# Performance work log

Measured on AMD Instinct MI355X. Metric: run time of the kernel, lower is better.

## Reference

```python
import jax, jax.numpy as jnp
import numpy as np

DIM = 256
RATIO = 4
SCALE = 8
B, H, W = 16, 128, 128
EPS = 1e-5


def _conv(x, w, pad):
    return jax.lax.conv_general_dilated(
        x, w, window_strides=(1, 1), padding=[(pad, pad), (pad, pad)],
        dimension_numbers=('NCHW', 'OIHW', 'NCHW'))


def _haar_dwt(x):
    # pywt.dwt2(x, 'haar') on even-sized inputs == strided 2x2 sum/difference
    a = x[:, :, 0::2, 0::2]
    b = x[:, :, 0::2, 1::2]
    c = x[:, :, 1::2, 0::2]
    d = x[:, :, 1::2, 1::2]
    ll = (a + b + c + d) * 0.5
    lh = (a + b - c - d) * 0.5  # cH: high-pass along rows
    hl = (a - b + c - d) * 0.5  # cV: high-pass along cols
    hh = (a - b - c + d) * 0.5  # cD
    return jnp.concatenate([ll, lh, hl, hh], axis=1)


def setup_inputs() -> dict:
    key = jax.random.key(0)
    ks = jax.random.split(key, 16)
    dq = DIM // RATIO
    ds = DIM // SCALE
    s = 0.05
    return {
        'x': jax.random.normal(ks[0], (B, DIM, H, W), jnp.float32),
        'reduce_w': jax.random.normal(ks[1], (dq, DIM, 1, 1), jnp.float32) * s,
        'reduce_b': jnp.zeros((dq,), jnp.float32),
        'bn_g': jnp.ones((dq,), jnp.float32),
        'bn_b': jnp.zeros((dq,), jnp.float32),
        'bn_mean': jnp.zeros((dq,), jnp.float32),
        'bn_var': jnp.ones((dq,), jnp.float32),
        'conv_w': jax.random.normal(ks[2], (1, DIM, 1, 1), jnp.float32) * s,
        'conv1_w': jax.random.normal(ks[3], (DIM, DIM, 1, 1), jnp.float32) * s,
        'conv2_w': jax.random.normal(ks[4], (DIM, DIM, 3, 3), jnp.float32) * s,
        'conv3_w': jax.random.normal(ks[5], (DIM, DIM, 5, 5), jnp.float32) * s,
        'conv4_w': jax.random.normal(ks[6], (DIM, DIM, 7, 7), jnp.float32) * s,
        'channel_conv_w': jax.random.normal(ks[7], (DIM, DIM, 3, 3), jnp.float32) * s,
        'conv1x1_w': jax.random.normal(ks[8], (DIM, 6 * DIM, 3, 3), jnp.float32) * s,
        'ct1_w': jax.random.normal(ks[9], (ds, DIM, 1, 1), jnp.float32) * s,
        'ct1_b': jnp.zeros((ds,), jnp.float32),
        'ln_g': jnp.ones((ds,), jnp.float32),
        'ln_b': jnp.zeros((ds,), jnp.float32),
        'ct2_w': jax.random.normal(ks[10], (DIM, ds, 1, 1), jnp.float32) * s,
        'ct2_b': jnp.zeros((DIM,), jnp.float32),
        'proj_w': jax.random.normal(ks[11], (DIM, DIM, 1, 1), jnp.float32) * s,
    }


def reference(x, reduce_w, reduce_b, bn_g, bn_b, bn_mean, bn_var, conv_w,
              conv1_w, conv2_w, conv3_w, conv4_w, channel_conv_w, conv1x1_w,
              ct1_w, ct1_b, ln_g, ln_b, ct2_w, ct2_b, proj_w):
    # max-pool 2x2 stride 2
    p = jax.lax.reduce_window(x, -jnp.inf, jax.lax.max,
                              (1, 1, 2, 2), (1, 1, 2, 2), 'VALID')
    # reduce: 1x1 conv -> BN (inference) -> ReLU
    r = _conv(x, reduce_w, 0) + reduce_b[None, :, None, None]
    r = (r - bn_mean[None, :, None, None]) * jax.lax.rsqrt(bn_var + EPS)[None, :, None, None]
    r = jax.nn.relu(r * bn_g[None, :, None, None] + bn_b[None, :, None, None])
    # Haar DWT (original runs under no_grad: detached from autograd)
    qkv0 = jax.lax.stop_gradient(_haar_dwt(r))  # [B, DIM, H/2, W/2]
    qkv1 = _conv(qkv0, conv1_w, 0)
    qkv2 = _conv(qkv0, conv2_w, 1)
    qkv3 = _conv(qkv0, conv3_w, 2)
    qkv4 = _conv(qkv0, conv4_w, 3)
    qkv = _conv(jnp.concatenate([qkv0, qkv1, qkv2, qkv3, qkv4, p], axis=1),
                conv1x1_w, 1)  # [B, DIM, H/2, W/2]
    n = (H // 2) * (W // 2)
    # spatial attention weights: softmax over spatial positions
    content = _conv(qkv, conv_w, 0).reshape(B, n)          # [B, N]
    content = jax.nn.softmax(content, axis=1)
    channel = _conv(qkv, channel_conv_w, 1).reshape(B, DIM, n)  # [B, C, N]
    pooled = jnp.einsum('bcn,bn->bc', channel, content)[:, :, None, None]
    # channel transform: 1x1 -> LayerNorm over (C,1,1) -> ReLU -> 1x1
    t = _conv(pooled, ct1_w, 0) + ct1_b[None, :, None, None]
    mu = jnp.mean(t, axis=(1, 2, 3), keepdims=True)
    var = jnp.mean(jnp.square(t - mu), axis=(1, 2, 3), keepdims=True)
    t = (t - mu) * jax.lax.rsqrt(var + EPS)
    t = jax.nn.relu(t * ln_g[None, :, None, None] + ln_b[None, :, None, None])
    cw = _conv(t, ct2_w, 0) + ct2_b[None, :, None, None]  # [B, DIM, 1, 1]
    return _conv(qkv * cw, proj_w, 0)
```

## Files before the change

kernel.cpp:

```cpp
#include <hip/hip_runtime.h>
#include <stdint.h>


typedef __attribute__((ext_vector_type(8))) short bf16x8;
typedef __attribute__((ext_vector_type(4))) float f32x4;

#define EPS_ 1e-5f

#define GLOAD16(gp, lp)                                                        \
  __builtin_amdgcn_global_load_lds(                                            \
      (const __attribute__((address_space(1))) void*)(gp),                     \
      (__attribute__((address_space(3))) void*)(lp), 16, 0, 0)

__device__ __forceinline__ float bf2f(unsigned short u) {
  union { unsigned int u; float f; } c; c.u = ((unsigned int)u) << 16; return c.f;
}
__device__ __forceinline__ unsigned short f2bf(float f) {
  union { float f; unsigned int u; } c; c.f = f;
  return (unsigned short)((c.u + 0x7fffu + ((c.u >> 16) & 1u)) >> 16);
}
__device__ __forceinline__ void unpack8(uint4 v, float* f) {
  f[0]=bf2f((unsigned short)(v.x&0xffffu)); f[1]=bf2f((unsigned short)(v.x>>16));
  f[2]=bf2f((unsigned short)(v.y&0xffffu)); f[3]=bf2f((unsigned short)(v.y>>16));
  f[4]=bf2f((unsigned short)(v.z&0xffffu)); f[5]=bf2f((unsigned short)(v.z>>16));
  f[6]=bf2f((unsigned short)(v.w&0xffffu)); f[7]=bf2f((unsigned short)(v.w>>16));
}
__device__ __forceinline__ uint4 pack8(const float* f) {
  uint4 v;
  v.x = (unsigned)f2bf(f[0]) | ((unsigned)f2bf(f[1])<<16);
  v.y = (unsigned)f2bf(f[2]) | ((unsigned)f2bf(f[3])<<16);
  v.z = (unsigned)f2bf(f[4]) | ((unsigned)f2bf(f[5])<<16);
  v.w = (unsigned)f2bf(f[6]) | ((unsigned)f2bf(f[7])<<16);
  return v;
}

__global__ void k_repack(const float* __restrict__ src, unsigned short* __restrict__ dst,
                         int O, int Opad, int I, int T) {
  int gid = blockIdx.x * 256 + threadIdx.x;
  if (gid >= Opad * I * T) return;
  int i = gid % I; int r = gid / I; int o = r % Opad; int t = r / Opad;
  dst[gid] = (o < O) ? f2bf(src[((size_t)(o * I + i)) * T + t]) : (unsigned short)0;
}

__global__ void k_fold1(const float* __restrict__ catw, const float* __restrict__ w1,
                        unsigned short* __restrict__ dst) {
  int gid = blockIdx.x; int tid = threadIdx.x;
  int iq = gid % 5; int o = (gid / 5) & 255; int t = gid / 1280;
  int i = iq * 256 + tid;
  float s;
  if (i < 256) {
    s = catw[((size_t)o * 1536 + i) * 9 + t];
    const float* cw = catw + ((size_t)o * 1536 + 256) * 9 + t;
    for (int m = 0; m < 256; ++m)
      s += cw[(size_t)m * 9] * w1[m * 256 + i];
  } else {
    s = catw[((size_t)o * 1536 + i + 256) * 9 + t];
  }
  dst[((size_t)t * 256 + o) * 1280 + i] = f2bf(s);
}

__global__ void k_border_zero(unsigned short* __restrict__ buf, int PW, int PB, int C) {
  int IW = PW - 2 * PB;
  int nb = PW * PW - IW * IW;
  int per = C >> 3;
  int gid = blockIdx.x * 256 + threadIdx.x;
  if (gid >= 16 * nb * per) return;
  int cq = gid % per; int r = gid / per; int p = r % nb; int b = r / nb;
  int y, x;
  int top = PB * PW;
  if (p < top) { y = p / PW; x = p - y * PW; }
  else if (p < top + IW * 2 * PB) {
    int q = p - top; y = PB + q / (2 * PB); int rr = q % (2 * PB);
    x = (rr < PB) ? rr : (IW + rr);
  } else { int q = p - top - IW * 2 * PB; y = PB + IW + q / PW; x = q - (q / PW) * PW; }
  uint4 z; z.x = z.y = z.z = z.w = 0u;
  *(uint4*)&buf[(((size_t)b * PW + y) * PW + x) * C + cq * 8] = z;
}

__global__ void k_transpose_x(const float* __restrict__ x, unsigned short* __restrict__ xh) {
  int by = blockIdx.x; int b = by >> 7; int y = by & 127;
  int tid = threadIdx.x;
  __shared__ unsigned short lds[32 * 129];
  for (int c0 = 0; c0 < 256; c0 += 32) {
    #pragma unroll
    for (int i = 0; i < 16; ++i) {
      int e = i * 256 + tid; int ci = e >> 7, xx = e & 127;
      float v = x[(((size_t)b * 256 + c0 + ci) * 128 + y) * 128 + xx];
      lds[ci * 129 + xx] = f2bf(v);
    }
    __syncthreads();
    #pragma unroll
    for (int i2 = 0; i2 < 2; ++i2) {
      int e = i2 * 256 + tid; int pix = e >> 2, q = e & 3;
      unsigned int w0, w1, w2, w3;
      w0 = (unsigned)lds[(q*8+0)*129 + pix] | ((unsigned)lds[(q*8+1)*129 + pix] << 16);
      w1 = (unsigned)lds[(q*8+2)*129 + pix] | ((unsigned)lds[(q*8+3)*129 + pix] << 16);
      w2 = (unsigned)lds[(q*8+4)*129 + pix] | ((unsigned)lds[(q*8+5)*129 + pix] << 16);
      w3 = (unsigned)lds[(q*8+6)*129 + pix] | ((unsigned)lds[(q*8+7)*129 + pix] << 16);
      uint4 v; v.x = w0; v.y = w1; v.z = w2; v.w = w3;
      *(uint4*)&xh[(((size_t)b * 128 + y) * 128 + pix) * 256 + c0 + q * 8] = v;
    }
    __syncthreads();
  }
}

__global__ void k_maxpool(const unsigned short* __restrict__ xh, unsigned short* __restrict__ cat) {
  int gid = blockIdx.x * 256 + threadIdx.x;
  int cq = gid & 31; int pix = gid >> 5;
  int bb = pix >> 12; int yx = pix & 4095;
  int y = yx >> 6, xx2 = yx & 63;
  size_t base = (((size_t)bb * 128 + 2 * y) * 128 + 2 * xx2) * 256 + cq * 8;
  uint4 v00 = *(const uint4*)(xh + base);
  uint4 v01 = *(const uint4*)(xh + base + 256);
  uint4 v10 = *(const uint4*)(xh + base + 32768);
  uint4 v11 = *(const uint4*)(xh + base + 32768 + 256);
  float a[8], b8[8], c8[8], d8[8], m8[8];
  unpack8(v00, a); unpack8(v01, b8); unpack8(v10, c8); unpack8(v11, d8);
  #pragma unroll
  for (int j = 0; j < 8; ++j) m8[j] = fmaxf(fmaxf(a[j], b8[j]), fmaxf(c8[j], d8[j]));
  *(uint4*)(cat + (((size_t)bb * 4900 + (y + 3) * 70 + (xx2 + 3))) * 1280 + 1024 + cq * 8) = pack8(m8);
}

__global__ void k_haar(const unsigned short* __restrict__ rbn, unsigned short* __restrict__ cat) {
  int gid = blockIdx.x * 256 + threadIdx.x;
  int cq = gid & 7; int pix = gid >> 3;
  int bb = pix >> 12; int yx = pix & 4095;
  int y = yx >> 6, xx = yx & 63;
  size_t base = (((size_t)bb * 128 + 2 * y) * 128 + 2 * xx) * 64 + cq * 8;
  uint4 va = *(const uint4*)(rbn + base);
  uint4 vb = *(const uint4*)(rbn + base + 64);
  uint4 vc = *(const uint4*)(rbn + base + 8192);
  uint4 vd = *(const uint4*)(rbn + base + 8192 + 64);
  float a[8], b8[8], c8[8], d8[8], o[8];
  unpack8(va, a); unpack8(vb, b8); unpack8(vc, c8); unpack8(vd, d8);
  size_t ob = ((size_t)bb * 4900 + (y + 3) * 70 + (xx + 3)) * 1280 + cq * 8;
  #pragma unroll
  for (int j = 0; j < 8; ++j) o[j] = (a[j] + b8[j] + c8[j] + d8[j]) * 0.5f;
  *(uint4*)(cat + ob + 0)   = pack8(o);
  #pragma unroll
  for (int j = 0; j < 8; ++j) o[j] = (a[j] + b8[j] - c8[j] - d8[j]) * 0.5f;
  *(uint4*)(cat + ob + 64)  = pack8(o);
  #pragma unroll
  for (int j = 0; j < 8; ++j) o[j] = (a[j] - b8[j] + c8[j] - d8[j]) * 0.5f;
  *(uint4*)(cat + ob + 128) = pack8(o);
  #pragma unroll
  for (int j = 0; j < 8; ++j) o[j] = (a[j] - b8[j] - c8[j] + d8[j]) * 0.5f;
  *(uint4*)(cat + ob + 192) = pack8(o);
}

__global__ __launch_bounds__(512, 1) void k_conv_gemm256(
    const unsigned short* __restrict__ Wt, const unsigned short* __restrict__ Bf,
    int Cin, int Cstr, int cbase,
    int PW, int PB, int KH, int pad,
    unsigned long long wbstride,
    unsigned short* __restrict__ outb, int OCstr, int ocbase, int OPW, int OPB,
    float* __restrict__ outf, int mode) {
  const int tid = threadIdx.x, lane = tid & 63, w = tid >> 6;
  const int wm = w >> 2, wn = w & 3;
  const int nidx = (blockIdx.x & 7) * 32 + (blockIdx.x >> 3);
  const int bn = (nidx & 15) * 256;
  const int b = nidx >> 4;
  if (wbstride) Wt += (size_t)b * wbstride;
  extern __shared__ unsigned short S[];

  f32x4 zero4 = {0.f, 0.f, 0.f, 0.f};
  f32x4 acc[8][4];
  #pragma unroll
  for (int i = 0; i < 8; ++i)
    #pragma unroll
    for (int j = 0; j < 4; ++j) acc[i][j] = zero4;

  const int lq = lane >> 3, lc = lane & 7;
  const int lg = (lc - lq) & 7;
  const int pr = lg >> 2;
  const int ks = lg & 3;
  const unsigned short* aSt = Wt + (size_t)(w * 32 + 2 * lq + pr) * Cin + ks * 8;
  const size_t jA = (size_t)16 * Cin;
  const size_t bimg = (size_t)b * PW * PW;
  const unsigned short* bSt0; const unsigned short* bSt1;
  {
    int p = bn + w * 32 + 2 * lq + pr;
    bSt0 = Bf + (bimg + (size_t)((p >> 6) + PB) * PW + ((p & 63) + PB)) * Cstr + cbase + ks * 8;
    p += 16;
    bSt1 = Bf + (bimg + (size_t)((p >> 6) + PB) * PW + ((p & 63) + PB)) * Cstr + cbase + ks * 8;
  }
  const int dA = w * 1024;
  const int dB = 8192 + w * 1024;

  const int r = lane & 15, s4 = lane >> 4;
  const int ck = (((r & 1) * 4 + s4) + ((r >> 1) & 7)) & 7;
  const int lb = (r >> 1) * 64 + ck * 8;
  const int aOff = wm * 4096 + lb;
  const int bOff = 8192 + wn * 2048 + lb;

  const size_t MC = (size_t)256 * Cin;
  const int NT = (KH * KH * Cin) >> 5;

  const long long t0B = ((long long)(-pad) * PW + (-pad)) * (long long)Cstr;
  GLOAD16(aSt,             S + dA);
  GLOAD16(aSt + jA,        S + dA + 512);
  GLOAD16(bSt0 + t0B,      S + dB);
  GLOAD16(bSt1 + t0B,      S + dB + 512);
  GLOAD16(aSt + 32,        S + 16384 + dA);
  GLOAD16(aSt + jA + 32,   S + 16384 + dA + 512);
  GLOAD16(bSt0 + t0B + 32, S + 16384 + dB);
  GLOAD16(bSt1 + t0B + 32, S + 16384 + dB + 512);
  asm volatile("s_waitcnt vmcnt(4)" ::: "memory");
  __builtin_amdgcn_s_barrier();
  __builtin_amdgcn_sched_barrier(0);

  int kc2 = 64, ty2 = 0, tx2 = 0;
  for (int t = 0; t < NT; ++t) {
    const unsigned short* Sc = S + (t & 3) * 16384;
    unsigned short* Sn = (unsigned short*)S + ((t + 2) & 3) * 16384;
    const bool hn = (t + 2) < NT;
    long long offA = 0, offB = 0;
    if (hn) {
      offA = (long long)(ty2 * KH + tx2) * MC + kc2;
      offB = ((long long)(ty2 - pad) * PW + (tx2 - pad)) * (long long)Cstr + kc2;
      kc2 += 32;
      if (kc2 == Cin) { kc2 = 0; ++tx2; if (tx2 == KH) { tx2 = 0; ++ty2; } }
    }
    bf16x8 a[4], bb[4];
    #pragma unroll
    for (int mi = 0; mi < 4; ++mi) a[mi] = *(const bf16x8*)(Sc + aOff + mi * 512);
    #pragma unroll
    for (int ni = 0; ni < 4; ++ni) bb[ni] = *(const bf16x8*)(Sc + bOff + ni * 512);
    if (hn) {
      GLOAD16(aSt + offA,      Sn + dA);
      GLOAD16(aSt + jA + offA, Sn + dA + 512);
    }
    __builtin_amdgcn_s_setprio(1);
    #pragma unroll
    for (int mi = 0; mi < 4; ++mi)
      #pragma unroll
      for (int ni = 0; ni < 4; ++ni)
        acc[mi][ni] = __builtin_amdgcn_mfma_f32_16x16x32_bf16(a[mi], bb[ni], acc[mi][ni], 0, 0, 0);
    __builtin_amdgcn_s_setprio(0);
    __builtin_amdgcn_s_barrier();
    #pragma unroll
    for (int mi = 0; mi < 4; ++mi) a[mi] = *(const bf16x8*)(Sc + aOff + (mi + 4) * 512);
    if (hn) {
      GLOAD16(bSt0 + offB, Sn + dB);
      GLOAD16(bSt1 + offB, Sn + dB + 512);
    }
    __builtin_amdgcn_s_setprio(1);
    #pragma unroll
    for (int mi = 0; mi < 4; ++mi)
      #pragma unroll
      for (int ni = 0; ni < 4; ++ni)
        acc[mi + 4][ni] = __builtin_amdgcn_mfma_f32_16x16x32_bf16(a[mi], bb[ni], acc[mi + 4][ni], 0, 0, 0);
    __builtin_amdgcn_s_setprio(0);
    if (t + 1 < NT) {
      if (t + 2 < NT) { asm volatile("s_waitcnt vmcnt(4)" ::: "memory"); }
      else            { asm volatile("s_waitcnt vmcnt(0)" ::: "memory"); }
      __builtin_amdgcn_s_barrier();
      __builtin_amdgcn_sched_barrier(0);
    }
  }

  const size_t bimgO = (size_t)b * OPW * OPW;
  #pragma unroll
  for (int mi = 0; mi < 8; ++mi) {
    const int mf = wm * 128 + mi * 16 + (lane >> 4) * 4;
    #pragma unroll
    for (int ni = 0; ni < 4; ++ni) {
      const int n = bn + wn * 64 + ni * 16 + (lane & 15);
      if (mode == 2) {
        #pragma unroll
        for (int vv = 0; vv < 4; ++vv)
          outf[((size_t)b * 256 + mf + vv) * 4096 + n] = acc[mi][ni][vv];
      } else {
        const int oy = n >> 6, ox = n & 63;
        unsigned short h[4];
        #pragma unroll
        for (int vv = 0; vv < 4; ++vv) h[vv] = f2bf(acc[mi][ni][vv]);
        uint2 st; st.x = (unsigned)h[0] | ((unsigned)h[1] << 16);
        st.y = (unsigned)h[2] | ((unsigned)h[3] << 16);
        *(uint2*)&outb[(bimgO + (size_t)(oy + OPB) * OPW + (ox + OPB)) * OCstr + ocbase + mf] = st;
      }
    }
  }
}

__global__ __launch_bounds__(256) void k_conv_gemm(
    const unsigned short* __restrict__ Wt, const unsigned short* __restrict__ Bf,
    int M, int Mpad, int Cin, int Cstr, int cbase,
    int OW, int lgOW, int PW, int PB, int KH, int pad,
    unsigned long long wbstride,
    unsigned short* __restrict__ outb, int OCstr, int ocbase, int OPW, int OPB,
    float* __restrict__ outf, int mode,
    const float* __restrict__ rb, const float* __restrict__ bng, const float* __restrict__ bnb,
    const float* __restrict__ bnm, const float* __restrict__ bnv) {
  const int tid = threadIdx.x, lane = tid & 63, w = tid >> 6;
  const int wm = w >> 1, wn = w & 1;
  const int bm = blockIdx.y * 128, bn = blockIdx.x * 128;
  const int b = blockIdx.z;
  const int Npix = OW * OW;
  if (wbstride) Wt += (size_t)b * wbstride;

  __shared__ __align__(1024) unsigned short sA[128 * 32];
  __shared__ __align__(1024) unsigned short sB[128 * 32];

  f32x4 zero4 = {0.f, 0.f, 0.f, 0.f};
  f32x4 acc[4][4];
  #pragma unroll
  for (int i = 0; i < 4; ++i)
    #pragma unroll
    for (int j = 0; j < 4; ++j) acc[i][j] = zero4;

  const int srow = lane >> 2;
  const int slog = (lane & 3) ^ ((lane >> 3) & 3);
  const int r0 = w * 32;
  const unsigned short* aRow = Wt + ((size_t)(bm + r0 + srow)) * Cin + slog * 8;
  const int n0 = bn + r0 + srow, n1 = n0 + 16;
  const int y0 = n0 >> lgOW, x0 = n0 & (OW - 1);
  const int y1 = n1 >> lgOW, x1 = n1 & (OW - 1);
  const size_t bimg = (size_t)b * PW * PW;
  const unsigned short* bRow0 = Bf + (bimg + (size_t)(y0 + PB) * PW + (x0 + PB)) * Cstr + cbase + slog * 8;
  const unsigned short* bRow1 = Bf + (bimg + (size_t)(y1 + PB) * PW + (x1 + PB)) * Cstr + cbase + slog * 8;
  unsigned short* ldsA0 = &sA[(r0) * 32];
  unsigned short* ldsA1 = &sA[(r0 + 16) * 32];
  unsigned short* ldsB0 = &sB[(r0) * 32];
  unsigned short* ldsB1 = &sB[(r0 + 16) * 32];

  const int rowfrag = lane & 15, hi = lane >> 4;
  const int sl = hi ^ ((rowfrag >> 1) & 3);
  const bf16x8* pA[4]; const bf16x8* pB[4];
  #pragma unroll
  for (int mi = 0; mi < 4; ++mi)
    pA[mi] = (const bf16x8*)&sA[(wm * 64 + mi * 16 + rowfrag) * 32 + sl * 8];
  #pragma unroll
  for (int ni = 0; ni < 4; ++ni)
    pB[ni] = (const bf16x8*)&sB[(wn * 64 + ni * 16 + rowfrag) * 32 + sl * 8];

  const size_t MC = (size_t)Mpad * Cin;
  for (int ty = 0; ty < KH; ++ty) {
    for (int tx = 0; tx < KH; ++tx) {
      const unsigned short* at = aRow + (size_t)(ty * KH + tx) * MC;
      const long long toff = ((long long)(ty - pad) * PW + (tx - pad)) * Cstr;
      const unsigned short* bt0 = bRow0 + toff;
      const unsigned short* bt1 = bRow1 + toff;
      for (int kc = 0; kc < Cin; kc += 32) {
        GLOAD16(at + kc, ldsA0);
        GLOAD16(at + (size_t)16 * Cin + kc, ldsA1);
        GLOAD16(bt0 + kc, ldsB0);
        GLOAD16(bt1 + kc, ldsB1);
        __syncthreads();
        bf16x8 af[4], bfr[4];
        #pragma unroll
        for (int mi = 0; mi < 4; ++mi) af[mi] = *pA[mi];
        #pragma unroll
        for (int ni = 0; ni < 4; ++ni) bfr[ni] = *pB[ni];
        #pragma unroll
        for (int mi = 0; mi < 4; ++mi)
          #pragma unroll
          for (int ni = 0; ni < 4; ++ni)
            acc[mi][ni] = __builtin_amdgcn_mfma_f32_16x16x32_bf16(af[mi], bfr[ni], acc[mi][ni], 0, 0, 0);
        __syncthreads();
      }
    }
  }

  const int mb0 = bm + wm * 64, nb0 = bn + wn * 64;
  const size_t bimgO = (size_t)b * OPW * OPW;
  #pragma unroll
  for (int mi = 0; mi < 4; ++mi) {
    const int mf = mb0 + mi * 16 + (lane >> 4) * 4;
    if (mf >= M) continue;
    #pragma unroll
    for (int ni = 0; ni < 4; ++ni) {
      const int n = nb0 + ni * 16 + (lane & 15);
      if (mode == 2) {
        #pragma unroll
        for (int vv = 0; vv < 4; ++vv)
          outf[((size_t)b * M + mf + vv) * Npix + n] = acc[mi][ni][vv];
      } else {
        const int oy = n >> lgOW, ox = n & (OW - 1);
        unsigned short h[4];
        #pragma unroll
        for (int vv = 0; vv < 4; ++vv) {
          float val = acc[mi][ni][vv];
          if (mode == 1) {
            int m = mf + vv;
            float scl = bng[m] * rsqrtf(bnv[m] + EPS_);
            val = (val + rb[m] - bnm[m]) * scl + bnb[m];
            val = fmaxf(val, 0.f);
          }
          h[vv] = f2bf(val);
        }
        uint2 st; st.x = (unsigned)h[0] | ((unsigned)h[1] << 16);
        st.y = (unsigned)h[2] | ((unsigned)h[3] << 16);
        *(uint2*)&outb[(bimgO + (size_t)(oy + OPB) * OPW + (ox + OPB)) * OCstr + ocbase + mf] = st;
      }
    }
  }
}

__global__ void k_content_logits(const unsigned short* __restrict__ qkv,
                                 const float* __restrict__ conv_w,
                                 float* __restrict__ logits) {
  int j = blockIdx.x, b = blockIdx.y, tid = threadIdx.x;
  __shared__ float wl[256];
  wl[tid] = conv_w[tid];
  __syncthreads();
  int pl = tid >> 3, kp = tid & 7;
  #pragma unroll
  for (int pass = 0; pass < 4; ++pass) {
    int p = j * 128 + pass * 32 + pl;
    int y = p >> 6, x = p & 63;
    const unsigned short* q = qkv + (((size_t)b * 66 + y + 1) * 66 + (x + 1)) * 256 + kp * 32;
    float s = 0.f;
    #pragma unroll
    for (int i = 0; i < 32; i += 8) {
      uint4 v = *(const uint4*)(q + i);
      float f[8]; unpack8(v, f);
      #pragma unroll
      for (int k = 0; k < 8; ++k) s += f[k] * wl[kp * 32 + i + k];
    }
    s += __shfl_down(s, 4, 8);
    s += __shfl_down(s, 2, 8);
    s += __shfl_down(s, 1, 8);
    if (kp == 0) logits[(size_t)b * 4096 + p] = s;
  }
}

__global__ void k_softmax4096(float* __restrict__ cont) {
  int b = blockIdx.x, tid = threadIdx.x;
  __shared__ float red[256];
  float sv[16]; float mx = -1e30f;
  #pragma unroll
  for (int j = 0; j < 16; ++j) { sv[j] = cont[(size_t)b * 4096 + j * 256 + tid]; mx = fmaxf(mx, sv[j]); }
  red[tid] = mx; __syncthreads();
  for (int s = 128; s > 0; s >>= 1) { if (tid < s) red[tid] = fmaxf(red[tid], red[tid + s]); __syncthreads(); }
  mx = red[0]; __syncthreads();
  float sum = 0.f;
  #pragma unroll
  for (int j = 0; j < 16; ++j) { sv[j] = expf(sv[j] - mx); sum += sv[j]; }
  red[tid] = sum; __syncthreads();
  for (int s = 128; s > 0; s >>= 1) { if (tid < s) red[tid] += red[tid + s]; __syncthreads(); }
  float inv = 1.f / red[0];
  #pragma unroll
  for (int j = 0; j < 16; ++j) cont[(size_t)b * 4096 + j * 256 + tid] = sv[j] * inv;
}

__global__ void k_corr(const unsigned short* __restrict__ qkv,
                       const float* __restrict__ cont, float* __restrict__ gpart) {
  int j = blockIdx.x, b = blockIdx.y, i = threadIdx.x;
  __shared__ float cl[640];
  for (int e = i; e < 640; e += 256) {
    int gy = j * 8 - 1 + (e >> 6);
    cl[e] = (gy >= 0 && gy < 64) ? cont[(size_t)b * 4096 + gy * 64 + (e & 63)] : 0.f;
  }
  __syncthreads();
  float g[9] = {0.f, 0.f, 0.f, 0.f, 0.f, 0.f, 0.f, 0.f, 0.f};
  for (int ry = 0; ry < 8; ++ry) {
    int y = j * 8 + ry;
    for (int x = 0; x < 64; ++x) {
      float qv = bf2f(qkv[(((size_t)b * 66 + y + 1) * 66 + (x + 1)) * 256 + i]);
      #pragma unroll
      for (int ky = 0; ky < 3; ++ky) {
        int ly = ry - ky + 2;
        #pragma unroll
        for (int kx = 0; kx < 3; ++kx) {
          int nx = x - kx + 1;
          if ((unsigned)nx < 64u) g[ky * 3 + kx] += qv * cl[ly * 64 + nx];
        }
      }
    }
  }
  size_t base = ((size_t)b * 8 + j) * 2304 + i;
  #pragma unroll
  for (int t = 0; t < 9; ++t) gpart[base + t * 256] = g[t];
}

__global__ void k_pooled_g(const float* __restrict__ gpart,
                           const float* __restrict__ wc, float* __restrict__ pooled) {
  int b = blockIdx.x, c = threadIdx.x;
  __shared__ float Gs[2304];
  for (int e = c; e < 2304; e += 256) {
    float s = 0.f;
    #pragma unroll
    for (int j = 0; j < 8; ++j) s += gpart[((size_t)b * 8 + j) * 2304 + e];
    Gs[e] = s;
  }
  __syncthreads();
  float acc = 0.f;
  const float* w = wc + (size_t)c * 2304;
  for (int i = 0; i < 256; ++i)
    #pragma unroll
    for (int t = 0; t < 9; ++t)
      acc += w[i * 9 + t] * Gs[t * 256 + i];
  pooled[b * 256 + c] = acc;
}

__global__ void k_ct(const float* __restrict__ pooled,
                     const float* __restrict__ ct1w, const float* __restrict__ ct1b,
                     const float* __restrict__ lng, const float* __restrict__ lnb,
                     const float* __restrict__ ct2w, const float* __restrict__ ct2b,
                     float* __restrict__ cw) {
  int b = blockIdx.x, tid = threadIdx.x;
  __shared__ float tt[32];
  __shared__ float stats[2];
  if (tid < 32) {
    float s = 0.f;
    const float* w = ct1w + tid * 256;
    const float* p = pooled + b * 256;
    for (int i = 0; i < 256; ++i) s += w[i] * p[i];
    tt[tid] = s + ct1b[tid];
  }
  __syncthreads();
  if (tid == 0) {
    float mu = 0.f;
    for (int j = 0; j < 32; ++j) mu += tt[j];
    mu *= (1.f / 32.f);
    float va = 0.f;
    for (int j = 0; j < 32; ++j) { float d = tt[j] - mu; va += d * d; }
    va *= (1.f / 32.f);
    stats[0] = mu; stats[1] = rsqrtf(va + EPS_);
  }
  __syncthreads();
  if (tid < 32) {
    float v = (tt[tid] - stats[0]) * stats[1];
    tt[tid] = fmaxf(v * lng[tid] + lnb[tid], 0.f);
  }
  __syncthreads();
  float s = 0.f;
  const float* w2 = ct2w + tid * 32;
  #pragma unroll
  for (int j = 0; j < 32; ++j) s += w2[j] * tt[j];
  cw[b * 256 + tid] = s + ct2b[tid];
}

__global__ void k_aproj(const float* __restrict__ projw, const float* __restrict__ cw,
                        unsigned short* __restrict__ aproj) {
  int gid = blockIdx.x * 256 + threadIdx.x;
  int b = gid >> 16; int oi = gid & 65535; int i = oi & 255;
  aproj[gid] = f2bf(projw[oi] * cw[b * 256 + i]);
}

extern "C" void kernel_launch(void* const* d_in, const int* in_sizes, int n_in,
                              void* d_out, int out_size, void* d_ws, size_t ws_size,
                              hipStream_t stream) {
  (void)in_sizes; (void)n_in; (void)out_size; (void)ws_size;
  const float* x        = (const float*)d_in[0];
  const float* reduce_w = (const float*)d_in[1];
  const float* reduce_b = (const float*)d_in[2];
  const float* bn_g     = (const float*)d_in[3];
  const float* bn_b     = (const float*)d_in[4];
  const float* bn_mean  = (const float*)d_in[5];
  const float* bn_var   = (const float*)d_in[6];
  const float* conv_w   = (const float*)d_in[7];
  const float* conv1_w  = (const float*)d_in[8];
  const float* conv2_w  = (const float*)d_in[9];
  const float* conv3_w  = (const float*)d_in[10];
  const float* conv4_w  = (const float*)d_in[11];
  const float* chconv_w = (const float*)d_in[12];
  const float* cat_w    = (const float*)d_in[13];
  const float* ct1_w    = (const float*)d_in[14];
  const float* ct1_b    = (const float*)d_in[15];
  const float* ln_g     = (const float*)d_in[16];
  const float* ln_b     = (const float*)d_in[17];
  const float* ct2_w    = (const float*)d_in[18];
  const float* ct2_b    = (const float*)d_in[19];
  const float* proj_w   = (const float*)d_in[20];

  static bool attr_done = false;
  if (!attr_done) {
    hipFuncSetAttribute(reinterpret_cast<const void*>(&k_conv_gemm256),
                        hipFuncAttributeMaxDynamicSharedMemorySize, 131072);
    attr_done = true;
  }

  char* wsp = (char*)d_ws;
  size_t off = 0;
  auto alloc = [&](size_t bytes) -> char* {
    char* p = wsp + off; off += (bytes + 255) & ~(size_t)255; return p;
  };
  unsigned short* XH    = (unsigned short*)alloc((size_t)16 * 16384 * 256 * 2);
  unsigned short* CAT   = (unsigned short*)alloc((size_t)16 * 4900 * 1280 * 2);
  unsigned short* RBN   = (unsigned short*)alloc((size_t)16 * 16384 * 64 * 2);
  unsigned short* QKV   = (unsigned short*)alloc((size_t)16 * 4356 * 256 * 2);
  float*          CONT  = (float*)alloc((size_t)16 * 4096 * 4);
  float*          GPART = (float*)alloc((size_t)16 * 8 * 2304 * 4);
  float*          POOL  = (float*)alloc(16 * 256 * 4);
  float*          CWB   = (float*)alloc(16 * 256 * 4);
  unsigned short* WR    = (unsigned short*)alloc((size_t)128 * 256 * 2);
  unsigned short* W2    = (unsigned short*)alloc((size_t)9 * 256 * 256 * 2);
  unsigned short* W3    = (unsigned short*)alloc((size_t)25 * 256 * 256 * 2);
  unsigned short* W4    = (unsigned short*)alloc((size_t)49 * 256 * 256 * 2);
  unsigned short* WBIG  = (unsigned short*)alloc((size_t)9 * 256 * 1280 * 2);
  unsigned short* APROJ = (unsigned short*)alloc((size_t)16 * 256 * 256 * 2);

  auto rp = [&](const float* s, unsigned short* d, int O, int Opad, int I, int T) {
    int tot = Opad * I * T;
    k_repack<<<(tot + 255) / 256, 256, 0, stream>>>(s, d, O, Opad, I, T);
  };
  rp(reduce_w, WR, 64, 128, 256, 1);
  rp(conv2_w, W2, 256, 256, 256, 9);
  rp(conv3_w, W3, 256, 256, 256, 25);
  rp(conv4_w, W4, 256, 256, 256, 49);
  k_fold1<<<9 * 256 * 5, 256, 0, stream>>>(cat_w, conv1_w, WBIG);

  k_border_zero<<<(16 * 804 * 160 + 255) / 256, 256, 0, stream>>>(CAT, 70, 3, 1280);
  k_border_zero<<<(16 * 260 * 32 + 255) / 256, 256, 0, stream>>>(QKV, 66, 1, 256);

  k_transpose_x<<<2048, 256, 0, stream>>>(x, XH);
  k_maxpool<<<8192, 256, 0, stream>>>(XH, CAT);

  dim3 blk(256);
  k_conv_gemm<<<dim3(128, 1, 16), blk, 0, stream>>>(WR, XH, 64, 128, 256, 256, 0,
      128, 7, 128, 0, 1, 0, 0ULL, RBN, 64, 0, 128, 0, nullptr, 1,
      reduce_b, bn_g, bn_b, bn_mean, bn_var);
  k_haar<<<2048, 256, 0, stream>>>(RBN, CAT);
  k_conv_gemm256<<<256, 512, 131072, stream>>>(W2, CAT, 256, 1280, 0,
      70, 3, 3, 1, 0ULL, CAT, 1280, 256, 70, 3, nullptr, 0);
  k_conv_gemm256<<<256, 512, 131072, stream>>>(W3, CAT, 256, 1280, 0,
      70, 3, 5, 2, 0ULL, CAT, 1280, 512, 70, 3, nullptr, 0);
  k_conv_gemm256<<<256, 512, 131072, stream>>>(W4, CAT, 256, 1280, 0,
      70, 3, 7, 3, 0ULL, CAT, 1280, 768, 70, 3, nullptr, 0);
  k_conv_gemm256<<<256, 512, 131072, stream>>>(WBIG, CAT, 1280, 1280, 0,
      70, 3, 3, 1, 0ULL, QKV, 256, 0, 66, 1, nullptr, 0);
  k_content_logits<<<dim3(32, 16), blk, 0, stream>>>(QKV, conv_w, CONT);
  k_softmax4096<<<16, blk, 0, stream>>>(CONT);
  k_corr<<<dim3(8, 16), blk, 0, stream>>>(QKV, CONT, GPART);
  k_pooled_g<<<16, blk, 0, stream>>>(GPART, chconv_w, POOL);
  k_ct<<<16, blk, 0, stream>>>(POOL, ct1_w, ct1_b, ln_g, ln_b, ct2_w, ct2_b, CWB);
  k_aproj<<<4096, 256, 0, stream>>>(proj_w, CWB, APROJ);
  k_conv_gemm256<<<256, 512, 131072, stream>>>(APROJ, QKV, 256, 256, 0,
      66, 1, 1, 0, 65536ULL, nullptr, 256, 0, 64, 0, (float*)d_out, 2);
}
```

Before: 1.599 ms.

## Parallelize spatial correlation per row and split pooled GEMV across blocks

The correlation kernel now launches one block per output row (64 per batch) instead of one per 8 rows, which gives 1024 blocks rather than 128 to fill the GPU. A new reduction kernel sums the 64 partial results. The pooled channel-conv GEMV is split over 16 channel groups per batch, with 16 threads per channel making coalesced weight reads and doing a shared-memory reduction. In exchange it adds a kernel launch and a larger partial buffer, and the three halo rows of the content map are reloaded for every row.

New measurement: 1.362 ms, median of 3. 14.8% less time.

```diff
diff --git a/kernel.cpp b/kernel.cpp
--- a/kernel.cpp
+++ b/kernel.cpp
@@ -447,51 +447,66 @@
 __global__ void k_corr(const unsigned short* __restrict__ qkv,
                        const float* __restrict__ cont, float* __restrict__ gpart) {
   int j = blockIdx.x, b = blockIdx.y, i = threadIdx.x;
-  __shared__ float cl[640];
-  for (int e = i; e < 640; e += 256) {
-    int gy = j * 8 - 1 + (e >> 6);
-    cl[e] = (gy >= 0 && gy < 64) ? cont[(size_t)b * 4096 + gy * 64 + (e & 63)] : 0.f;
+  __shared__ float cl[192];
+  if (i < 192) {
+    int gy = j - 1 + (i >> 6);
+    cl[i] = (gy >= 0 && gy < 64) ? cont[(size_t)b * 4096 + gy * 64 + (i & 63)] : 0.f;
   }
   __syncthreads();
   float g[9] = {0.f, 0.f, 0.f, 0.f, 0.f, 0.f, 0.f, 0.f, 0.f};
-  for (int ry = 0; ry < 8; ++ry) {
-    int y = j * 8 + ry;
-    for (int x = 0; x < 64; ++x) {
-      float qv = bf2f(qkv[(((size_t)b * 66 + y + 1) * 66 + (x + 1)) * 256 + i]);
+  const unsigned short* qrow = qkv + (((size_t)b * 66 + j + 1) * 66 + 1) * 256 + i;
+  for (int x = 0; x < 64; ++x) {
+    float qv = bf2f(qrow[(size_t)x * 256]);
+    #pragma unroll
+    for (int ky = 0; ky < 3; ++ky) {
+      const int ly = 2 - ky;
       #pragma unroll
-      for (int ky = 0; ky < 3; ++ky) {
-        int ly = ry - ky + 2;
-        #pragma unroll
-        for (int kx = 0; kx < 3; ++kx) {
-          int nx = x - kx + 1;
-          if ((unsigned)nx < 64u) g[ky * 3 + kx] += qv * cl[ly * 64 + nx];
-        }
+      for (int kx = 0; kx < 3; ++kx) {
+        int nx = x - kx + 1;
+        if ((unsigned)nx < 64u) g[ky * 3 + kx] += qv * cl[ly * 64 + nx];
       }
     }
   }
-  size_t base = ((size_t)b * 8 + j) * 2304 + i;
+  size_t base = ((size_t)b * 64 + j) * 2304 + i;
   #pragma unroll
   for (int t = 0; t < 9; ++t) gpart[base + t * 256] = g[t];
 }
 
-__global__ void k_pooled_g(const float* __restrict__ gpart,
+__global__ void k_gred(const float* __restrict__ gpart, float* __restrict__ gred) {
+  int gid = blockIdx.x * 256 + threadIdx.x;
+  if (gid >= 16 * 2304) return;
+  int b = gid / 2304, e = gid - b * 2304;
+  float s = 0.f;
+  const float* p = gpart + (size_t)b * 64 * 2304 + e;
+  for (int j = 0; j < 64; ++j) s += p[(size_t)j * 2304];
+  gred[gid] = s;
+}
+
+__global__ void k_pooled_g(const float* __restrict__ gred,
                            const float* __restrict__ wc, float* __restrict__ pooled) {
-  int b = blockIdx.x, c = threadIdx.x;
+  int cg = blockIdx.x, b = blockIdx.y;
+  int tid = threadIdx.x;
+  int cl_ = tid >> 4, part = tid & 15;
   __shared__ float Gs[2304];
-  for (int e = c; e < 2304; e += 256) {
+  __shared__ float red[256];
+  for (int e = tid; e < 2304; e += 256) {
+    int i = e / 9, t = e - i * 9;
+    Gs[e] = gred[(size_t)b * 2304 + t * 256 + i];
+  }
+  __syncthreads();
+  int c = cg * 16 + cl_;
+  const float* w = wc + (size_t)c * 2304 + part;
+  float acc = 0.f;
+  #pragma unroll 4
+  for (int q = 0; q < 144; ++q) acc += w[q * 16] * Gs[part + q * 16];
+  red[tid] = acc;
+  __syncthreads();
+  if (part == 0) {
     float s = 0.f;
     #pragma unroll
-    for (int j = 0; j < 8; ++j) s += gpart[((size_t)b * 8 + j) * 2304 + e];
-    Gs[e] = s;
-  }
-  __syncthreads();
-  float acc = 0.f;
-  const float* w = wc + (size_t)c * 2304;
-  for (int i = 0; i < 256; ++i)
-    #pragma unroll
-    for (int t = 0; t < 9; ++t)
-      acc += w[i * 9 + t] * Gs[t * 256 + i];
-  pooled[b * 256 + c] = acc;
+    for (int q = 0; q < 16; ++q) s += red[cl_ * 16 + q];
+    pooled[b * 256 + c] = s;
+  }
 }
 
 __global__ void k_ct(const float* __restrict__ pooled,
@@ -582,7 +597,8 @@
   unsigned short* RBN   = (unsigned short*)alloc((size_t)16 * 16384 * 64 * 2);
   unsigned short* QKV   = (unsigned short*)alloc((size_t)16 * 4356 * 256 * 2);
   float*          CONT  = (float*)alloc((size_t)16 * 4096 * 4);
-  float*          GPART = (float*)alloc((size_t)16 * 8 * 2304 * 4);
+  float*          GPART = (float*)alloc((size_t)16 * 64 * 2304 * 4);
+  float*          GRED  = (float*)alloc((size_t)16 * 2304 * 4);
   float*          POOL  = (float*)alloc(16 * 256 * 4);
   float*          CWB   = (float*)alloc(16 * 256 * 4);
   unsigned short* WR    = (unsigned short*)alloc((size_t)128 * 256 * 2);
@@ -623,8 +639,9 @@
       70, 3, 3, 1, 0ULL, QKV, 256, 0, 66, 1, nullptr, 0);
   k_content_logits<<<dim3(32, 16), blk, 0, stream>>>(QKV, conv_w, CONT);
   k_softmax4096<<<16, blk, 0, stream>>>(CONT);
-  k_corr<<<dim3(8, 16), blk, 0, stream>>>(QKV, CONT, GPART);
-  k_pooled_g<<<16, blk, 0, stream>>>(GPART, chconv_w, POOL);
+  k_corr<<<dim3(64, 16), blk, 0, stream>>>(QKV, CONT, GPART);
+  k_gred<<<144, blk, 0, stream>>>(GPART, GRED);
+  k_pooled_g<<<dim3(16, 16), blk, 0, stream>>>(GRED, chconv_w, POOL);
   k_ct<<<16, blk, 0, stream>>>(POOL, ct1_w, ct1_b, ln_g, ln_b, ct2_w, ct2_b, CWB);
   k_aproj<<<4096, 256, 0, stream>>>(proj_w, CWB, APROJ);
   k_conv_gemm256<<<256, 512, 131072, stream>>>(APROJ, QKV, 256, 256, 0,
```
